# Performance work log

Hardware: AMD Instinct MI355X
Metric: run time of the kernel (lower is better)

The kernel has to match this reference:

```python
import jax, jax.numpy as jnp
import numpy as np

B, L, D = 8192, 200, 64
NUM_ITEMS = 100000
HID = 64  # attention hidden_dim


def setup_inputs() -> dict:
    key = jax.random.key(0)
    ks = jax.random.split(key, 16)
    inp = {
        "item_sequence": jax.random.randint(ks[0], (B, L), 0, NUM_ITEMS),
        "click_sequence": jax.random.randint(ks[1], (B, L), 0, 2),
        "seq_length": jax.random.randint(ks[2], (B, 1), 1, L + 1),
        "target_item": jax.random.randint(ks[3], (B, 1), 0, NUM_ITEMS),
        "context_features": jax.random.normal(ks[4], (B, 9), dtype=jnp.float32),
        # embedding table (num_items+1, D)
        "emb_table": jax.random.normal(ks[5], (NUM_ITEMS + 1, D), dtype=jnp.float32) * 0.05,
        # attention MLP: Linear(2D->64), Linear(64->32), Linear(32->1)
        "aw1": jax.random.normal(ks[6], (2 * D, HID), dtype=jnp.float32) * 0.05,
        "ab1": jnp.zeros((HID,), jnp.float32),
        "aw2": jax.random.normal(ks[7], (HID, HID // 2), dtype=jnp.float32) * 0.05,
        "ab2": jnp.zeros((HID // 2,), jnp.float32),
        "aw3": jax.random.normal(ks[8], (HID // 2, 1), dtype=jnp.float32) * 0.05,
        "ab3": jnp.zeros((1,), jnp.float32),
        # context MLP: Linear(9->32)
        "cw": jax.random.normal(ks[9], (9, 32), dtype=jnp.float32) * 0.05,
        "cb": jnp.zeros((32,), jnp.float32),
        # head MLP: Linear(160->128), Linear(128->64), Linear(64->1)
        "mw1": jax.random.normal(ks[10], (2 * D + 32, 128), dtype=jnp.float32) * 0.05,
        "mb1": jnp.zeros((128,), jnp.float32),
        "mw2": jax.random.normal(ks[11], (128, 64), dtype=jnp.float32) * 0.05,
        "mb2": jnp.zeros((64,), jnp.float32),
        "mw3": jax.random.normal(ks[12], (64, 1), dtype=jnp.float32) * 0.05,
        "mb3": jnp.zeros((1,), jnp.float32),
    }
    return inp


def reference(item_sequence, click_sequence, seq_length, target_item, context_features,
              emb_table, aw1, ab1, aw2, ab2, aw3, ab3, cw, cb,
              mw1, mb1, mw2, mb2, mw3, mb3):
    seq_emb = emb_table[item_sequence]                 # [B, L, D]
    tgt_emb = emb_table[target_item[:, 0]]             # [B, D]
    seq_len = item_sequence.shape[1]
    mask = (jnp.arange(seq_len)[None, :] < seq_length).astype(seq_emb.dtype)  # [B, L]

    # DIN attention: concat(query, keys) -> 3-layer MLP -> masked softmax -> weighted sum
    q = jnp.broadcast_to(tgt_emb[:, None, :], seq_emb.shape)          # [B, L, D]
    att_in = jnp.concatenate([q, seq_emb], axis=-1)                   # [B, L, 2D]
    h = jax.nn.relu(att_in @ aw1 + ab1)
    h = jax.nn.relu(h @ aw2 + ab2)
    scores = (h @ aw3 + ab3)[..., 0]                                  # [B, L]
    scores = jnp.where(mask == 0, jnp.asarray(-1e9, scores.dtype), scores)
    w = jax.nn.softmax(scores, axis=1)                                # [B, L]
    attended = jnp.einsum('bl,bld->bd', w, seq_emb)                   # [B, D]

    ctx = jax.nn.relu(context_features @ cw + cb)                     # [B, 32]
    comb = jnp.concatenate([attended, tgt_emb, ctx], axis=1)          # [B, 2D+32]
    h = jax.nn.relu(comb @ mw1 + mb1)
    h = jax.nn.relu(h @ mw2 + mb2)
    out = jax.nn.sigmoid(h @ mw3 + mb3)[:, 0]                         # [B]
    return out
```

## Files before the change

### kernel.cpp

```cpp
#include <hip/hip_runtime.h>
#include <cmath>

typedef __attribute__((ext_vector_type(8))) short s16x8;
typedef __attribute__((ext_vector_type(4))) float f32x4;
typedef __attribute__((ext_vector_type(2))) float f32x2;

__device__ __forceinline__ short f2bf(float f) {
    union { float f; unsigned u; } v; v.f = f;
    unsigned r = v.u + 0x7FFFu + ((v.u >> 16) & 1u);
    return (short)(r >> 16);
}
__device__ __forceinline__ float bf2f(short s) {
    union { unsigned u; float f; } v; v.u = ((unsigned)(unsigned short)s) << 16;
    return v.f;
}
__device__ __forceinline__ unsigned cvtpk2(float lo, float hi) {
    unsigned r;
    asm("v_cvt_pk_bf16_f32 %0, %1, %2" : "=v"(r) : "v"(lo), "v"(hi));
    return r;
}
__device__ __forceinline__ s16x8 cvt8(float4 a, float4 b) {
    union { s16x8 v; unsigned u[4]; } r;
    r.u[0] = cvtpk2(a.x, a.y);
    r.u[1] = cvtpk2(a.z, a.w);
    r.u[2] = cvtpk2(b.x, b.y);
    r.u[3] = cvtpk2(b.z, b.w);
    return r.v;
}
__device__ __forceinline__ float rsum16(float x) {
    int t;
    t = __builtin_amdgcn_update_dpp(0, __builtin_bit_cast(int, x), 0x108, 0xF, 0xF, true);
    x += __builtin_bit_cast(float, t);
    t = __builtin_amdgcn_update_dpp(0, __builtin_bit_cast(int, x), 0x104, 0xF, 0xF, true);
    x += __builtin_bit_cast(float, t);
    t = __builtin_amdgcn_update_dpp(0, __builtin_bit_cast(int, x), 0x102, 0xF, 0xF, true);
    x += __builtin_bit_cast(float, t);
    t = __builtin_amdgcn_update_dpp(0, __builtin_bit_cast(int, x), 0x101, 0xF, 0xF, true);
    x += __builtin_bit_cast(float, t);
    return x;
}

#define W1SEQ_SH  0
#define W2_SH     8192
#define MW1T_SH   10240
#define MW2T_SH   30720
#define QC_F      19456
#define CB_SH     1087488
#define EMB_SH    2400256
#define EMB_ROWS  100001
#define EMB_VEC8  800008

__global__ __launch_bounds__(256)
void din_prep_kernel(const int* __restrict__ tgt_item,
                     const float* __restrict__ emb,
                     const float* __restrict__ ab1,
                     const float* __restrict__ aw1,
                     const float* __restrict__ aw2,
                     const float* __restrict__ mw1,
                     const float* __restrict__ mw2,
                     short* __restrict__ ws)
{
    const int t = threadIdx.x;
    if (blockIdx.x < 128) {
        const int lane = t & 63, wave = t >> 6;
        const int quad = lane >> 4, r16 = lane & 15;
        float* qc = (float*)ws + QC_F;

        const int b0 = (blockIdx.x * 4 + wave) * 16;
        const int it = tgt_item[b0 + r16];
        const float* rp = emb + (size_t)it * 64 + quad * 8;
        float4 v0 = *(const float4*)(rp),      v1 = *(const float4*)(rp + 4);
        float4 v2 = *(const float4*)(rp + 32), v3 = *(const float4*)(rp + 36);
        s16x8 a0 = cvt8(v0, v1);
        s16x8 a1 = cvt8(v2, v3);

        f32x4 acc[4] = {{0,0,0,0},{0,0,0,0},{0,0,0,0},{0,0,0,0}};
        #pragma unroll
        for (int nt = 0; nt < 4; ++nt) {
            const float* colp = aw1 + nt * 16 + r16;
            s16x8 b_0, b_1;
            #pragma unroll
            for (int j = 0; j < 8; ++j) {
                b_0[j] = f2bf(colp[(quad * 8 + j) * 64]);
                b_1[j] = f2bf(colp[(32 + quad * 8 + j) * 64]);
            }
            acc[nt] = __builtin_amdgcn_mfma_f32_16x16x32_bf16(a0, b_0, acc[nt], 0, 0, 0);
            acc[nt] = __builtin_amdgcn_mfma_f32_16x16x32_bf16(a1, b_1, acc[nt], 0, 0, 0);
        }
        #pragma unroll
        for (int nt = 0; nt < 4; ++nt) {
            float bias = ab1[nt * 16 + r16];
            #pragma unroll
            for (int rr = 0; rr < 4; ++rr)
                qc[(b0 + quad * 4 + rr) * 64 + nt * 16 + r16] = acc[nt][rr] + bias;
        }
        return;
    }
    if (blockIdx.x >= 192) {
        const int idx = (blockIdx.x - 192) * 256 + t;
        if (idx < EMB_VEC8) {
            const float* rp = emb + (size_t)idx * 8;
            float4 v0 = *(const float4*)(rp);
            float4 v1 = *(const float4*)(rp + 4);
            *(s16x8*)(ws + EMB_SH + (size_t)idx * 8) = cvt8(v0, v1);
        }
        return;
    }
    const int bb = blockIdx.x - 128;
    const int g  = bb >> 3;
    const int sb = bb & 7;
    if (g == 0) {
        for (int idx = sb * 512 + t; idx < sb * 512 + 512; idx += 256) {
            int j = idx & 7, lane = (idx >> 3) & 63, fr = idx >> 9;
            int n = (fr >> 1) * 16 + (lane & 15);
            int k = (fr & 1) * 32 + (lane >> 4) * 8 + j;
            ws[W1SEQ_SH + idx] = f2bf(aw1[(64 + k) * 64 + n]);
        }
    } else if (g == 1) {
    } else if (g == 2) {
        int idx = sb * 256 + t;
        int j = idx & 7, lane = (idx >> 3) & 63, fr = idx >> 9;
        int n = (fr >> 1) * 16 + (lane & 15);
        int k = (fr & 1) * 32 + (lane >> 4) * 8 + j;
        ws[W2_SH + idx] = f2bf(aw2[k * 32 + n]);
    } else if (g == 3) {
        for (int idx = sb * 1024 + t; idx < sb * 1024 + 1024; idx += 256) {
            int j = idx & 7, lane = (idx >> 3) & 63, fr = idx >> 9;
            int n = (fr >> 2) * 16 + (lane & 15);
            int k = (fr & 3) * 32 + (lane >> 4) * 8 + j;
            ws[MW2T_SH + idx] = f2bf(mw2[k * 64 + n]);
        }
    } else {
        const int base = ((g - 4) * 8 + sb) * 640;
        for (int ii = t; ii < 640; ii += 256) {
            int idx = base + ii;
            int j = idx & 7, lane = (idx >> 3) & 63, fr = idx >> 9;
            int nt = fr / 5, ks = fr - nt * 5;
            int n = nt * 16 + (lane & 15);
            int k = ks * 32 + (lane >> 4) * 8 + j;
            ws[MW1T_SH + idx] = f2bf(mw1[k * 128 + n]);
        }
    }
}

#define H1_PITCH 72
template<bool TAB>
__global__ __launch_bounds__(256)
void din_att_v7(const int* __restrict__ item_seq,
                const int* __restrict__ seq_len_p,
                const int* __restrict__ tgt_item,
                const float* __restrict__ ctx_feat,
                const float* __restrict__ emb,
                const float* __restrict__ ab2,
                const float* __restrict__ aw3, const float* __restrict__ ab3,
                const float* __restrict__ cw,  const float* __restrict__ cb,
                short* __restrict__ ws)
{
    const int t = threadIdx.x, lane = t & 63, wave = t >> 6;
    const int quad = lane >> 4, r16 = lane & 15;
    __shared__ short s_w1[4096];
    __shared__ short s_h1[4][16 * H1_PITCH];
    __shared__ float s_sc[4][64];
    __shared__ float s_pool[4][64];
    __shared__ float s_m[4], s_e[4];

    const int b   = blockIdx.x;
    const int len = seq_len_p[b];
    const int tgt = tgt_item[b];

    {
        const s16x8* src = (const s16x8*)(ws + W1SEQ_SH);
        s16x8* dst = (s16x8*)s_w1;
        dst[t]       = src[t];
        dst[t + 256] = src[t + 256];
    }

    bool act[4];
    s16x8 af[4][2];
    #pragma unroll
    for (int ci = 0; ci < 4; ++ci) {
        const int c = wave + ci * 4;
        act[ci] = (c < 13) && (c * 16 < len);
        if (act[ci]) {
            int r = c * 16 + r16; if (r > 199) r = 199;
            const int it = item_seq[b * 200 + r];
            if constexpr (TAB) {
                const short* rp = ws + EMB_SH + (size_t)it * 64 + quad * 8;
                af[ci][0] = *(const s16x8*)(rp);
                af[ci][1] = *(const s16x8*)(rp + 32);
            } else {
                const float* rp = emb + (size_t)it * 64 + quad * 8;
                float4 v0 = *(const float4*)(rp),      v1 = *(const float4*)(rp + 4);
                float4 v2 = *(const float4*)(rp + 32), v3 = *(const float4*)(rp + 36);
                af[ci][0] = cvt8(v0, v1);
                af[ci][1] = cvt8(v2, v3);
            }
        }
    }
    s16x8 w2r[4];
    #pragma unroll
    for (int fr = 0; fr < 4; ++fr)
        w2r[fr] = *(const s16x8*)(ws + W2_SH + (fr * 64 + lane) * 8);
    const float* qcp = (const float*)ws + QC_F + b * 64;
    float qcv[4];
    #pragma unroll
    for (int nt = 0; nt < 4; ++nt) qcv[nt] = qcp[nt * 16 + r16];
    const float bias2_lo = ab2[r16], bias2_hi = ab2[16 + r16];
    const float w3_lo    = aw3[r16], w3_hi    = aw3[16 + r16];
    const float b3       = ab3[0];
    __syncthreads();

    short* h1w = s_h1[wave];

    #pragma unroll
    for (int ci = 0; ci < 4; ++ci) {
        if (!act[ci]) continue;
        f32x4 acc[4] = {{0,0,0,0},{0,0,0,0},{0,0,0,0},{0,0,0,0}};
        __builtin_amdgcn_s_setprio(1);
        #pragma unroll
        for (int nt = 0; nt < 4; ++nt) {
            s16x8 b_0 = *(const s16x8*)&s_w1[((nt * 2 + 0) * 64 + lane) * 8];
            s16x8 b_1 = *(const s16x8*)&s_w1[((nt * 2 + 1) * 64 + lane) * 8];
            acc[nt] = __builtin_amdgcn_mfma_f32_16x16x32_bf16(af[ci][0], b_0, acc[nt], 0, 0, 0);
            acc[nt] = __builtin_amdgcn_mfma_f32_16x16x32_bf16(af[ci][1], b_1, acc[nt], 0, 0, 0);
        }
        __builtin_amdgcn_s_setprio(0);
        #pragma unroll
        for (int nt = 0; nt < 4; ++nt) {
            float v0 = fmaxf(acc[nt][0] + qcv[nt], 0.f);
            float v1 = fmaxf(acc[nt][1] + qcv[nt], 0.f);
            float v2 = fmaxf(acc[nt][2] + qcv[nt], 0.f);
            float v3 = fmaxf(acc[nt][3] + qcv[nt], 0.f);
            unsigned p01 = cvtpk2(v0, v1), p23 = cvtpk2(v2, v3);
            const int col = nt * 16 + r16;
            h1w[(quad * 4 + 0) * H1_PITCH + col] = (short)p01;
            h1w[(quad * 4 + 1) * H1_PITCH + col] = (short)(p01 >> 16);
            h1w[(quad * 4 + 2) * H1_PITCH + col] = (short)p23;
            h1w[(quad * 4 + 3) * H1_PITCH + col] = (short)(p23 >> 16);
        }
        __builtin_amdgcn_wave_barrier();

        s16x8 h0  = *(const s16x8*)&h1w[r16 * H1_PITCH + quad * 8];
        s16x8 h1v = *(const s16x8*)&h1w[r16 * H1_PITCH + 32 + quad * 8];
        f32x4 c2[2] = {{0,0,0,0},{0,0,0,0}};
        __builtin_amdgcn_s_setprio(1);
        #pragma unroll
        for (int nt = 0; nt < 2; ++nt) {
            c2[nt] = __builtin_amdgcn_mfma_f32_16x16x32_bf16(h0,  w2r[nt * 2],     c2[nt], 0, 0, 0);
            c2[nt] = __builtin_amdgcn_mfma_f32_16x16x32_bf16(h1v, w2r[nt * 2 + 1], c2[nt], 0, 0, 0);
        }
        __builtin_amdgcn_s_setprio(0);
        #pragma unroll
        for (int rr = 0; rr < 4; ++rr) {
            float p = fmaxf(c2[0][rr] + bias2_lo, 0.f) * w3_lo
                    + fmaxf(c2[1][rr] + bias2_hi, 0.f) * w3_hi;
            p = rsum16(p);
            if (r16 == 0) s_sc[wave][ci * 16 + quad * 4 + rr] = p + b3;
        }
        __builtin_amdgcn_wave_barrier();
    }

    const int ci_l = lane >> 4;
    const int c_l  = wave + ci_l * 4;
    const int grow = c_l * 16 + r16;
    const bool valid = (c_l < 13) && (grow < len);
    float sc = valid ? s_sc[wave][lane] : -1e30f;
    float m = sc;
    #pragma unroll
    for (int off = 32; off; off >>= 1) m = fmaxf(m, __shfl_xor(m, off));
    float wgt = valid ? __expf(sc - m) : 0.f;
    float e = wgt;
    #pragma unroll
    for (int off = 32; off; off >>= 1) e += __shfl_xor(e, off);
    s_sc[wave][lane] = wgt;
    __builtin_amdgcn_wave_barrier();

    f32x2 p2[8];
    #pragma unroll
    for (int i = 0; i < 8; ++i) p2[i] = (f32x2){0.f, 0.f};
    #pragma unroll
    for (int ci = 0; ci < 4; ++ci) {
        if (!act[ci]) continue;
        const float w = s_sc[wave][ci * 16 + r16];
        const f32x2 w2 = {w, w};
        union { s16x8 v; unsigned u[4]; } a0, a1;
        a0.v = af[ci][0]; a1.v = af[ci][1];
        #pragma unroll
        for (int mi = 0; mi < 4; ++mi) {
            f32x2 e0, e1;
            e0[0] = __builtin_bit_cast(float, a0.u[mi] << 16);
            e0[1] = __builtin_bit_cast(float, a0.u[mi] & 0xFFFF0000u);
            e1[0] = __builtin_bit_cast(float, a1.u[mi] << 16);
            e1[1] = __builtin_bit_cast(float, a1.u[mi] & 0xFFFF0000u);
            p2[mi]     += w2 * e0;
            p2[4 + mi] += w2 * e1;
        }
    }
    float pr[16];
    #pragma unroll
    for (int mi = 0; mi < 4; ++mi) {
        pr[2 * mi]         = rsum16(p2[mi][0]);
        pr[2 * mi + 1]     = rsum16(p2[mi][1]);
        pr[8 + 2 * mi]     = rsum16(p2[4 + mi][0]);
        pr[8 + 2 * mi + 1] = rsum16(p2[4 + mi][1]);
    }
    if (r16 == 0) {
        #pragma unroll
        for (int j = 0; j < 8; ++j) {
            s_pool[wave][quad * 8 + j]      = pr[j];
            s_pool[wave][32 + quad * 8 + j] = pr[8 + j];
        }
    }
    if (lane == 0) { s_m[wave] = m; s_e[wave] = e; }
    __syncthreads();

    short* comb = ws + CB_SH + b * 160;
    if (t < 64) {
        float gm = fmaxf(fmaxf(s_m[0], s_m[1]), fmaxf(s_m[2], s_m[3]));
        float s0 = __expf(s_m[0] - gm), s1 = __expf(s_m[1] - gm);
        float s2 = __expf(s_m[2] - gm), s3 = __expf(s_m[3] - gm);
        float denom = s0 * s_e[0] + s1 * s_e[1] + s2 * s_e[2] + s3 * s_e[3];
        float pooled = s0 * s_pool[0][t] + s1 * s_pool[1][t]
                     + s2 * s_pool[2][t] + s3 * s_pool[3][t];
        comb[t] = f2bf(pooled / denom);
    } else if (t < 96) {
        const int j = t - 64;
        float a = cb[j];
        #pragma unroll
        for (int k = 0; k < 9; ++k) a += ctx_feat[b * 9 + k] * cw[k * 32 + j];
        comb[128 + j] = f2bf(fmaxf(a, 0.f));
    } else if (t < 160) {
        if constexpr (TAB) {
            comb[64 + (t - 96)] = ws[EMB_SH + (size_t)tgt * 64 + (t - 96)];
        } else {
            comb[64 + (t - 96)] = f2bf(emb[(size_t)tgt * 64 + (t - 96)]);
        }
    }
}

__global__ __launch_bounds__(256)
void din_mlp_kernel(const float* __restrict__ mb1,
                    const float* __restrict__ mb2,
                    const float* __restrict__ mw3, const float* __restrict__ mb3,
                    const short* __restrict__ ws,
                    float* __restrict__ out)
{
    const int t = threadIdx.x, lane = t & 63, wave = t >> 6;
    const int quad = lane >> 4, r16 = lane & 15;
    __shared__ short s_h1[16 * 136];
    __shared__ short s_h2[16 * 72];

    const int b0 = blockIdx.x * 16;
    const short* comb = ws + CB_SH;
    const short* w1   = ws + MW1T_SH;
    const short* w2   = ws + MW2T_SH;

    s16x8 a[5];
    #pragma unroll
    for (int ks = 0; ks < 5; ++ks)
        a[ks] = *(const s16x8*)(comb + (b0 + r16) * 160 + ks * 32 + quad * 8);
    f32x4 acc[2] = {{0,0,0,0},{0,0,0,0}};
    #pragma unroll
    for (int ntl = 0; ntl < 2; ++ntl) {
        const int nt = wave * 2 + ntl;
        #pragma unroll
        for (int ks = 0; ks < 5; ++ks) {
            s16x8 bf = *(const s16x8*)(w1 + ((nt * 5 + ks) * 64 + lane) * 8);
            acc[ntl] = __builtin_amdgcn_mfma_f32_16x16x32_bf16(a[ks], bf, acc[ntl], 0, 0, 0);
        }
    }
    #pragma unroll
    for (int ntl = 0; ntl < 2; ++ntl) {
        const int nt = wave * 2 + ntl;
        float bias = mb1[nt * 16 + r16];
        float v0 = fmaxf(acc[ntl][0] + bias, 0.f);
        float v1 = fmaxf(acc[ntl][1] + bias, 0.f);
        float v2 = fmaxf(acc[ntl][2] + bias, 0.f);
        float v3 = fmaxf(acc[ntl][3] + bias, 0.f);
        unsigned p01 = cvtpk2(v0, v1), p23 = cvtpk2(v2, v3);
        const int col = nt * 16 + r16;
        s_h1[(quad * 4 + 0) * 136 + col] = (short)p01;
        s_h1[(quad * 4 + 1) * 136 + col] = (short)(p01 >> 16);
        s_h1[(quad * 4 + 2) * 136 + col] = (short)p23;
        s_h1[(quad * 4 + 3) * 136 + col] = (short)(p23 >> 16);
    }
    __syncthreads();

    s16x8 a2[4];
    #pragma unroll
    for (int ks = 0; ks < 4; ++ks)
        a2[ks] = *(const s16x8*)&s_h1[r16 * 136 + ks * 32 + quad * 8];
    f32x4 acc2 = {0,0,0,0};
    {
        const int nt = wave;
        #pragma unroll
        for (int ks = 0; ks < 4; ++ks) {
            s16x8 bf = *(const s16x8*)(w2 + ((nt * 4 + ks) * 64 + lane) * 8);
            acc2 = __builtin_amdgcn_mfma_f32_16x16x32_bf16(a2[ks], bf, acc2, 0, 0, 0);
        }
        float bias = mb2[nt * 16 + r16];
        float v0 = fmaxf(acc2[0] + bias, 0.f);
        float v1 = fmaxf(acc2[1] + bias, 0.f);
        float v2 = fmaxf(acc2[2] + bias, 0.f);
        float v3 = fmaxf(acc2[3] + bias, 0.f);
        unsigned p01 = cvtpk2(v0, v1), p23 = cvtpk2(v2, v3);
        const int col = nt * 16 + r16;
        s_h2[(quad * 4 + 0) * 72 + col] = (short)p01;
        s_h2[(quad * 4 + 1) * 72 + col] = (short)(p01 >> 16);
        s_h2[(quad * 4 + 2) * 72 + col] = (short)p23;
        s_h2[(quad * 4 + 3) * 72 + col] = (short)(p23 >> 16);
    }
    __syncthreads();

    if (wave == 0) {
        float p = 0.f;
        #pragma unroll
        for (int j = 0; j < 16; ++j)
            p += bf2f(s_h2[r16 * 72 + quad * 16 + j]) * mw3[quad * 16 + j];
        p += __shfl_xor(p, 16);
        p += __shfl_xor(p, 32);
        if (quad == 0) out[b0 + r16] = 1.f / (1.f + __expf(-(p + mb3[0])));
    }
}

extern "C" void kernel_launch(void* const* d_in, const int* in_sizes, int n_in,
                              void* d_out, int out_size, void* d_ws, size_t ws_size,
                              hipStream_t stream)
{
    const int*   item_seq  = (const int*)  d_in[0];
    const int*   seq_len   = (const int*)  d_in[2];
    const int*   tgt_item  = (const int*)  d_in[3];
    const float* ctx_feat  = (const float*)d_in[4];
    const float* emb       = (const float*)d_in[5];
    const float* aw1 = (const float*)d_in[6];
    const float* ab1 = (const float*)d_in[7];
    const float* aw2 = (const float*)d_in[8];
    const float* ab2 = (const float*)d_in[9];
    const float* aw3 = (const float*)d_in[10];
    const float* ab3 = (const float*)d_in[11];
    const float* cw  = (const float*)d_in[12];
    const float* cb  = (const float*)d_in[13];
    const float* mw1 = (const float*)d_in[14];
    const float* mb1 = (const float*)d_in[15];
    const float* mw2 = (const float*)d_in[16];
    const float* mb2 = (const float*)d_in[17];
    const float* mw3 = (const float*)d_in[18];
    const float* mb3 = (const float*)d_in[19];
    float* out = (float*)d_out;
    short* ws  = (short*)d_ws;

    const size_t need_bytes = (size_t)(EMB_SH + EMB_ROWS * 64) * sizeof(short);
    const bool tab = ws_size >= need_bytes;

    if (tab) {
        hipLaunchKernelGGL(din_prep_kernel, dim3(128 + 64 + 3126), dim3(256), 0, stream,
                           tgt_item, emb, ab1, aw1, aw2, mw1, mw2, ws);
        hipLaunchKernelGGL(din_att_v7<true>, dim3(8192), dim3(256), 0, stream,
                           item_seq, seq_len, tgt_item, ctx_feat, emb,
                           ab2, aw3, ab3, cw, cb, ws);
    } else {
        hipLaunchKernelGGL(din_prep_kernel, dim3(128 + 64), dim3(256), 0, stream,
                           tgt_item, emb, ab1, aw1, aw2, mw1, mw2, ws);
        hipLaunchKernelGGL(din_att_v7<false>, dim3(8192), dim3(256), 0, stream,
                           item_seq, seq_len, tgt_item, ctx_feat, emb,
                           ab2, aw3, ab3, cw, cb, ws);
    }
    hipLaunchKernelGGL(din_mlp_kernel, dim3(512), dim3(256), 0, stream,
                       mb1, mb2, mw3, mb3, ws, out);
}
```

Baseline: 161.3 us.

## Fuse head MLP into attention kernel via last-block-per-group atomic counter

```diff
diff --git a/kernel.cpp b/kernel.cpp
--- a/kernel.cpp
+++ b/kernel.cpp
@@ -46,6 +46,7 @@
 #define MW2T_SH   30720
 #define QC_F      19456
 #define CB_SH     1087488
+#define CNT_SH    2398208
 #define EMB_SH    2400256
 #define EMB_ROWS  100001
 #define EMB_VEC8  800008
@@ -117,6 +118,7 @@
             ws[W1SEQ_SH + idx] = f2bf(aw1[(64 + k) * 64 + n]);
         }
     } else if (g == 1) {
+        if (sb < 2) ((int*)(ws + CNT_SH))[sb * 256 + t] = 0;
     } else if (g == 2) {
         int idx = sb * 256 + t;
         int j = idx & 7, lane = (idx >> 3) & 63, fr = idx >> 9;
@@ -146,7 +148,7 @@
 #define H1_PITCH 72
 template<bool TAB>
 __global__ __launch_bounds__(256)
-void din_att_v7(const int* __restrict__ item_seq,
+void din_att_v8(const int* __restrict__ item_seq,
                 const int* __restrict__ seq_len_p,
                 const int* __restrict__ tgt_item,
                 const float* __restrict__ ctx_feat,
@@ -154,7 +156,10 @@
                 const float* __restrict__ ab2,
                 const float* __restrict__ aw3, const float* __restrict__ ab3,
                 const float* __restrict__ cw,  const float* __restrict__ cb,
-                short* __restrict__ ws)
+                const float* __restrict__ mb1, const float* __restrict__ mb2,
+                const float* __restrict__ mw3, const float* __restrict__ mb3,
+                short* __restrict__ ws,
+                float* __restrict__ out)
 {
     const int t = threadIdx.x, lane = t & 63, wave = t >> 6;
     const int quad = lane >> 4, r16 = lane & 15;
@@ -163,6 +168,9 @@
     __shared__ float s_sc[4][64];
     __shared__ float s_pool[4][64];
     __shared__ float s_m[4], s_e[4];
+    __shared__ short s_mh1[16 * 136];
+    __shared__ short s_mh2[16 * 72];
+    __shared__ int   s_last;
 
     const int b   = blockIdx.x;
     const int len = seq_len_p[b];
@@ -216,7 +224,6 @@
     for (int ci = 0; ci < 4; ++ci) {
         if (!act[ci]) continue;
         f32x4 acc[4] = {{0,0,0,0},{0,0,0,0},{0,0,0,0},{0,0,0,0}};
-        __builtin_amdgcn_s_setprio(1);
         #pragma unroll
         for (int nt = 0; nt < 4; ++nt) {
             s16x8 b_0 = *(const s16x8*)&s_w1[((nt * 2 + 0) * 64 + lane) * 8];
@@ -224,7 +231,6 @@
             acc[nt] = __builtin_amdgcn_mfma_f32_16x16x32_bf16(af[ci][0], b_0, acc[nt], 0, 0, 0);
             acc[nt] = __builtin_amdgcn_mfma_f32_16x16x32_bf16(af[ci][1], b_1, acc[nt], 0, 0, 0);
         }
-        __builtin_amdgcn_s_setprio(0);
         #pragma unroll
         for (int nt = 0; nt < 4; ++nt) {
             float v0 = fmaxf(acc[nt][0] + qcv[nt], 0.f);
@@ -243,13 +249,11 @@
         s16x8 h0  = *(const s16x8*)&h1w[r16 * H1_PITCH + quad * 8];
         s16x8 h1v = *(const s16x8*)&h1w[r16 * H1_PITCH + 32 + quad * 8];
         f32x4 c2[2] = {{0,0,0,0},{0,0,0,0}};
-        __builtin_amdgcn_s_setprio(1);
         #pragma unroll
         for (int nt = 0; nt < 2; ++nt) {
             c2[nt] = __builtin_amdgcn_mfma_f32_16x16x32_bf16(h0,  w2r[nt * 2],     c2[nt], 0, 0, 0);
             c2[nt] = __builtin_amdgcn_mfma_f32_16x16x32_bf16(h1v, w2r[nt * 2 + 1], c2[nt], 0, 0, 0);
         }
-        __builtin_amdgcn_s_setprio(0);
         #pragma unroll
         for (int rr = 0; rr < 4; ++rr) {
             float p = fmaxf(c2[0][rr] + bias2_lo, 0.f) * w3_lo
@@ -336,90 +340,88 @@
             comb[64 + (t - 96)] = f2bf(emb[(size_t)tgt * 64 + (t - 96)]);
         }
     }
-}
-
-__global__ __launch_bounds__(256)
-void din_mlp_kernel(const float* __restrict__ mb1,
-                    const float* __restrict__ mb2,
-                    const float* __restrict__ mw3, const float* __restrict__ mb3,
-                    const short* __restrict__ ws,
-                    float* __restrict__ out)
-{
-    const int t = threadIdx.x, lane = t & 63, wave = t >> 6;
-    const int quad = lane >> 4, r16 = lane & 15;
-    __shared__ short s_h1[16 * 136];
-    __shared__ short s_h2[16 * 72];
-
-    const int b0 = blockIdx.x * 16;
-    const short* comb = ws + CB_SH;
-    const short* w1   = ws + MW1T_SH;
-    const short* w2   = ws + MW2T_SH;
-
-    s16x8 a[5];
-    #pragma unroll
-    for (int ks = 0; ks < 5; ++ks)
-        a[ks] = *(const s16x8*)(comb + (b0 + r16) * 160 + ks * 32 + quad * 8);
-    f32x4 acc[2] = {{0,0,0,0},{0,0,0,0}};
-    #pragma unroll
-    for (int ntl = 0; ntl < 2; ++ntl) {
-        const int nt = wave * 2 + ntl;
-        #pragma unroll
-        for (int ks = 0; ks < 5; ++ks) {
-            s16x8 bf = *(const s16x8*)(w1 + ((nt * 5 + ks) * 64 + lane) * 8);
-            acc[ntl] = __builtin_amdgcn_mfma_f32_16x16x32_bf16(a[ks], bf, acc[ntl], 0, 0, 0);
-        }
-    }
-    #pragma unroll
-    for (int ntl = 0; ntl < 2; ++ntl) {
-        const int nt = wave * 2 + ntl;
-        float bias = mb1[nt * 16 + r16];
-        float v0 = fmaxf(acc[ntl][0] + bias, 0.f);
-        float v1 = fmaxf(acc[ntl][1] + bias, 0.f);
-        float v2 = fmaxf(acc[ntl][2] + bias, 0.f);
-        float v3 = fmaxf(acc[ntl][3] + bias, 0.f);
-        unsigned p01 = cvtpk2(v0, v1), p23 = cvtpk2(v2, v3);
-        const int col = nt * 16 + r16;
-        s_h1[(quad * 4 + 0) * 136 + col] = (short)p01;
-        s_h1[(quad * 4 + 1) * 136 + col] = (short)(p01 >> 16);
-        s_h1[(quad * 4 + 2) * 136 + col] = (short)p23;
-        s_h1[(quad * 4 + 3) * 136 + col] = (short)(p23 >> 16);
-    }
+
     __syncthreads();
-
-    s16x8 a2[4];
-    #pragma unroll
-    for (int ks = 0; ks < 4; ++ks)
-        a2[ks] = *(const s16x8*)&s_h1[r16 * 136 + ks * 32 + quad * 8];
-    f32x4 acc2 = {0,0,0,0};
-    {
-        const int nt = wave;
-        #pragma unroll
-        for (int ks = 0; ks < 4; ++ks) {
-            s16x8 bf = *(const s16x8*)(w2 + ((nt * 4 + ks) * 64 + lane) * 8);
-            acc2 = __builtin_amdgcn_mfma_f32_16x16x32_bf16(a2[ks], bf, acc2, 0, 0, 0);
-        }
-        float bias = mb2[nt * 16 + r16];
-        float v0 = fmaxf(acc2[0] + bias, 0.f);
-        float v1 = fmaxf(acc2[1] + bias, 0.f);
-        float v2 = fmaxf(acc2[2] + bias, 0.f);
-        float v3 = fmaxf(acc2[3] + bias, 0.f);
-        unsigned p01 = cvtpk2(v0, v1), p23 = cvtpk2(v2, v3);
-        const int col = nt * 16 + r16;
-        s_h2[(quad * 4 + 0) * 72 + col] = (short)p01;
-        s_h2[(quad * 4 + 1) * 72 + col] = (short)(p01 >> 16);
-        s_h2[(quad * 4 + 2) * 72 + col] = (short)p23;
-        s_h2[(quad * 4 + 3) * 72 + col] = (short)(p23 >> 16);
+    if (t == 0) {
+        __threadfence();
+        int* cnt = (int*)(ws + CNT_SH);
+        int old = atomicAdd(&cnt[b >> 4], 1);
+        s_last = (old == 15) ? 1 : 0;
+        if (old == 15) __threadfence();
     }
     __syncthreads();
-
-    if (wave == 0) {
-        float p = 0.f;
-        #pragma unroll
-        for (int j = 0; j < 16; ++j)
-            p += bf2f(s_h2[r16 * 72 + quad * 16 + j]) * mw3[quad * 16 + j];
-        p += __shfl_xor(p, 16);
-        p += __shfl_xor(p, 32);
-        if (quad == 0) out[b0 + r16] = 1.f / (1.f + __expf(-(p + mb3[0])));
+    if (s_last) {
+        const int g16 = (b >> 4) * 16;
+        const short* combg = ws + CB_SH + (size_t)g16 * 160;
+        const short* w1p   = ws + MW1T_SH;
+        const short* w2p   = ws + MW2T_SH;
+
+        s16x8 am[5];
+        #pragma unroll
+        for (int ks = 0; ks < 5; ++ks)
+            am[ks] = *(const s16x8*)(combg + r16 * 160 + ks * 32 + quad * 8);
+        f32x4 macc[2] = {{0,0,0,0},{0,0,0,0}};
+        #pragma unroll
+        for (int ntl = 0; ntl < 2; ++ntl) {
+            const int nt = wave * 2 + ntl;
+            #pragma unroll
+            for (int ks = 0; ks < 5; ++ks) {
+                s16x8 bf = *(const s16x8*)(w1p + ((nt * 5 + ks) * 64 + lane) * 8);
+                macc[ntl] = __builtin_amdgcn_mfma_f32_16x16x32_bf16(am[ks], bf, macc[ntl], 0, 0, 0);
+            }
+        }
+        #pragma unroll
+        for (int ntl = 0; ntl < 2; ++ntl) {
+            const int nt = wave * 2 + ntl;
+            float bias = mb1[nt * 16 + r16];
+            float v0 = fmaxf(macc[ntl][0] + bias, 0.f);
+            float v1 = fmaxf(macc[ntl][1] + bias, 0.f);
+            float v2 = fmaxf(macc[ntl][2] + bias, 0.f);
+            float v3 = fmaxf(macc[ntl][3] + bias, 0.f);
+            unsigned p01 = cvtpk2(v0, v1), p23 = cvtpk2(v2, v3);
+            const int col = nt * 16 + r16;
+            s_mh1[(quad * 4 + 0) * 136 + col] = (short)p01;
+            s_mh1[(quad * 4 + 1) * 136 + col] = (short)(p01 >> 16);
+            s_mh1[(quad * 4 + 2) * 136 + col] = (short)p23;
+            s_mh1[(quad * 4 + 3) * 136 + col] = (short)(p23 >> 16);
+        }
+        __syncthreads();
+
+        s16x8 a2[4];
+        #pragma unroll
+        for (int ks = 0; ks < 4; ++ks)
+            a2[ks] = *(const s16x8*)&s_mh1[r16 * 136 + ks * 32 + quad * 8];
+        f32x4 acc2 = {0,0,0,0};
+        {
+            const int nt = wave;
+            #pragma unroll
+            for (int ks = 0; ks < 4; ++ks) {
+                s16x8 bf = *(const s16x8*)(w2p + ((nt * 4 + ks) * 64 + lane) * 8);
+                acc2 = __builtin_amdgcn_mfma_f32_16x16x32_bf16(a2[ks], bf, acc2, 0, 0, 0);
+            }
+            float bias = mb2[nt * 16 + r16];
+            float v0 = fmaxf(acc2[0] + bias, 0.f);
+            float v1 = fmaxf(acc2[1] + bias, 0.f);
+            float v2 = fmaxf(acc2[2] + bias, 0.f);
+            float v3 = fmaxf(acc2[3] + bias, 0.f);
+            unsigned p01 = cvtpk2(v0, v1), p23 = cvtpk2(v2, v3);
+            const int col = nt * 16 + r16;
+            s_mh2[(quad * 4 + 0) * 72 + col] = (short)p01;
+            s_mh2[(quad * 4 + 1) * 72 + col] = (short)(p01 >> 16);
+            s_mh2[(quad * 4 + 2) * 72 + col] = (short)p23;
+            s_mh2[(quad * 4 + 3) * 72 + col] = (short)(p23 >> 16);
+        }
+        __syncthreads();
+
+        if (wave == 0) {
+            float p = 0.f;
+            #pragma unroll
+            for (int j = 0; j < 16; ++j)
+                p += bf2f(s_mh2[r16 * 72 + quad * 16 + j]) * mw3[quad * 16 + j];
+            p += __shfl_xor(p, 16);
+            p += __shfl_xor(p, 32);
+            if (quad == 0) out[g16 + r16] = 1.f / (1.f + __expf(-(p + mb3[0])));
+        }
     }
 }
 
@@ -455,16 +457,14 @@
     if (tab) {
         hipLaunchKernelGGL(din_prep_kernel, dim3(128 + 64 + 3126), dim3(256), 0, stream,
                            tgt_item, emb, ab1, aw1, aw2, mw1, mw2, ws);
-        hipLaunchKernelGGL(din_att_v7<true>, dim3(8192), dim3(256), 0, stream,
+        hipLaunchKernelGGL(din_att_v8<true>, dim3(8192), dim3(256), 0, stream,
                            item_seq, seq_len, tgt_item, ctx_feat, emb,
-                           ab2, aw3, ab3, cw, cb, ws);
+                           ab2, aw3, ab3, cw, cb, mb1, mb2, mw3, mb3, ws, out);
     } else {
         hipLaunchKernelGGL(din_prep_kernel, dim3(128 + 64), dim3(256), 0, stream,
                            tgt_item, emb, ab1, aw1, aw2, mw1, mw2, ws);
-        hipLaunchKernelGGL(din_att_v7<false>, dim3(8192), dim3(256), 0, stream,
+        hipLaunchKernelGGL(din_att_v8<false>, dim3(8192), dim3(256), 0, stream,
                            item_seq, seq_len, tgt_item, ctx_feat, emb,
-                           ab2, aw3, ab3, cw, cb, ws);
-    }
-    hipLaunchKernelGGL(din_mlp_kernel, dim3(512), dim3(256), 0, stream,
-                       mb1, mb2, mw3, mb3, ws, out);
-}
+                           ab2, aw3, ab3, cw, cb, mb1, mb2, mw3, mb3, ws, out);
+    }
+}
```

Result: slower. 426.6 us (+164.5%).
